# Kernel tuning notes

Hardware: AMD Instinct MI355X
Metric: run time of the kernel (lower is better)

Reference implementation:

```python
import jax, jax.numpy as jnp
import numpy as np

N = 100000   # nodes
E = 1000000  # edges
H = 64       # hidden_channels
METAPATH = (0, 1, 2)


def setup_inputs() -> dict:
    key = jax.random.key(0)
    ks = jax.random.split(key, 32)
    inp = {
        "x": jax.random.normal(ks[0], (N, 2 * H), dtype=jnp.float32),
        "edge_index": jax.random.randint(ks[1], (2, E), 0, N, dtype=jnp.int64),
        "edge_type": jax.random.randint(ks[2], (E,), 0, 3, dtype=jnp.int64),
    }
    # layer 0: in = 2H, layers 1,2: in = H; torch Linear weight is [out, in]
    ki = 3
    for l, in_dim in enumerate([2 * H, H, H]):
        for wname in ["wl", "w0", "w1"]:
            inp[f"{wname}{l}"] = jax.random.normal(ks[ki], (H, in_dim), dtype=jnp.float32) * 0.05
            ki += 1
            inp[f"{wname[0]}b{wname[1]}{l}"] = jnp.zeros((H,), dtype=jnp.float32)
    return inp


def _layer(x_in, h, mask, src, dst, wl, bl, w0, b0, w1, b1):
    # aggr='add', flow='target_to_source': agg[src[e]] += h[dst[e]] for masked edges
    msg = jnp.where(mask[:, None], h[dst], jnp.zeros((), h.dtype))  # [E, H]
    agg = jax.ops.segment_sum(msg, src, num_segments=N)             # [N, H]
    return agg @ wl.T + bl + h @ w0.T + b0 + x_in @ w1.T + b1


def reference(x, edge_index, edge_type,
              wl0, wbl0, w00, wb00, w10, wb10,
              wl1, wbl1, w01, wb01, w11, wb11,
              wl2, wbl2, w02, wb02, w12, wb12):
    src, dst = edge_index[0], edge_index[1]
    params = [
        (wl0, wbl0, w00, wb00, w10, wb10),
        (wl1, wbl1, w01, wb01, w11, wb11),
        (wl2, wbl2, w02, wb02, w12, wb12),
    ]
    h = x
    for i, rel in enumerate(METAPATH):
        mask = edge_type == rel
        x_in = x if i == 0 else h
        h = jax.nn.relu(_layer(x_in, h, mask, src, dst, *params[i]))
        # F.dropout with training=False is identity (eval mode reference)
    return h
```

## Files before the change

### kernel.cpp

```cpp
#include <hip/hip_runtime.h>
#include <cstdint>
#include <cstddef>

#define NNODES 100000
#define NEDGES 1000000
#define NREL 3
#define RN (NREL * NNODES)
#define EPB 2048
#define SCAN_BLOCKS ((RN + EPB - 1) / EPB)


__global__ __launch_bounds__(256) void hist_kernel(
    const int* __restrict__ srcv, const int* __restrict__ ety, int* __restrict__ cnt)
{
    const int e = (int)(blockIdx.x * 256 + threadIdx.x);
    if (e < NEDGES) atomicAdd(&cnt[ety[e] * NNODES + srcv[e]], 1);
}

__global__ __launch_bounds__(256) void scan_reduce(
    const int* __restrict__ cnt, int* __restrict__ bsum)
{
    __shared__ int sd[256];
    const int t = (int)threadIdx.x;
    const int base = (int)blockIdx.x * EPB + t * 8;
    int s = 0;
    #pragma unroll
    for (int i = 0; i < 8; ++i)
        if (base + i < RN) s += cnt[base + i];
    sd[t] = s;
    __syncthreads();
    for (int st = 128; st > 0; st >>= 1) {
        if (t < st) sd[t] += sd[t + st];
        __syncthreads();
    }
    if (t == 0) bsum[blockIdx.x] = sd[0];
}

__global__ __launch_bounds__(256) void scan_blocksums(int* __restrict__ bsum, int nb)
{
    __shared__ int buf0[256], buf1[256];
    const int t = (int)threadIdx.x;
    buf0[t] = (t < nb) ? bsum[t] : 0;
    __syncthreads();
    int* a = buf0; int* b = buf1;
    for (int st = 1; st < 256; st <<= 1) {
        int v = a[t];
        if (t >= st) v += a[t - st];
        b[t] = v;
        __syncthreads();
        int* tmp = a; a = b; b = tmp;
    }
    if (t < nb) bsum[t] = (t == 0) ? 0 : a[t - 1];
}

__global__ __launch_bounds__(256) void scan_final(
    const int* __restrict__ cnt, const int* __restrict__ bsum,
    int* __restrict__ off, int* __restrict__ wptr)
{
    __shared__ int buf0[256], buf1[256];
    const int t = (int)threadIdx.x;
    const int base = (int)blockIdx.x * EPB + t * 8;
    int v[8];
    int tot = 0;
    #pragma unroll
    for (int i = 0; i < 8; ++i) {
        v[i] = (base + i < RN) ? cnt[base + i] : 0;
        tot += v[i];
    }
    buf0[t] = tot;
    __syncthreads();
    int* a = buf0; int* b = buf1;
    for (int st = 1; st < 256; st <<= 1) {
        int s = a[t];
        if (t >= st) s += a[t - st];
        b[t] = s;
        __syncthreads();
        int* tmp = a; a = b; b = tmp;
    }
    int o = bsum[blockIdx.x] + ((t == 0) ? 0 : a[t - 1]);
    #pragma unroll
    for (int i = 0; i < 8; ++i) {
        if (base + i < RN) { off[base + i] = o; wptr[base + i] = o; }
        o += v[i];
    }
    if (blockIdx.x == 0 && t == 0) off[RN] = NEDGES;
}

__global__ __launch_bounds__(256) void fill_kernel(
    const int* __restrict__ srcv, const int* __restrict__ dstv,
    const int* __restrict__ ety, int* __restrict__ wptr, int* __restrict__ ebuf)
{
    const int e = (int)(blockIdx.x * 256 + threadIdx.x);
    if (e < NEDGES) {
        const int pos = atomicAdd(&wptr[ety[e] * NNODES + srcv[e]], 1);
        ebuf[pos] = dstv[e];
    }
}

template<int K>
__global__ __launch_bounds__(256) void gather_kernel(
    const int* __restrict__ off, const int* __restrict__ ebuf,
    const float* __restrict__ h, float* __restrict__ agg, int rel)
{
    const int lane = (int)(threadIdx.x & 63);
    const int wid  = (int)((blockIdx.x * blockDim.x + threadIdx.x) >> 6);
    const int nw   = (int)((gridDim.x * blockDim.x) >> 6);
    const int* o = off + rel * NNODES;
    for (int n = wid; n < NNODES; n += nw) {
        const int s  = o[n];
        const int e1 = o[n + 1];
        float a0 = 0.f, a1 = 0.f;
        for (int j = s; j < e1; ++j) {
            const int d = ebuf[j];
            const float* hr = h + (size_t)d * K;
            a0 += hr[lane];
            if (K == 128) a1 += hr[64 + lane];
        }
        agg[(size_t)n * K + lane] = a0;
        if (K == 128) agg[(size_t)n * K + 64 + lane] = a1;
    }
}

template<int K>
__global__ __launch_bounds__(256) void dense_gemm(
    const float* __restrict__ A1, const float* __restrict__ A2,
    const float* __restrict__ W1, const float* __restrict__ W2a, const float* __restrict__ W2b,
    const float* __restrict__ B1, const float* __restrict__ B2, const float* __restrict__ B3,
    float* __restrict__ out, int nNodes)
{
    __shared__ float As[16][64];
    __shared__ float Ws[16][64];

    const int t  = (int)threadIdx.x;
    const int tx = t & 15;
    const int ty = t >> 4;
    const int n0 = (int)blockIdx.x * 64;

    const int srow = t >> 2;
    const int skk  = (t & 3) * 4;

    float4 acc[4];
    #pragma unroll
    for (int i = 0; i < 4; ++i) acc[i] = make_float4(0.f, 0.f, 0.f, 0.f);

    const int KC = K / 16;
    const int nA = n0 + srow;

    #pragma unroll 1
    for (int c = 0; c < 2 * KC; ++c) {
        const bool first = (c < KC);
        const int k0 = (first ? c : c - KC) * 16;

        float4 av = make_float4(0.f, 0.f, 0.f, 0.f);
        if (nA < nNodes) {
            const float* Ab = first ? A1 : A2;
            av = *(const float4*)(Ab + (size_t)nA * K + k0 + skk);
        }
        float4 wv;
        if (first) {
            wv = *(const float4*)(W1 + (size_t)srow * K + k0 + skk);
        } else {
            const float4 a = *(const float4*)(W2a + (size_t)srow * K + k0 + skk);
            const float4 b = *(const float4*)(W2b + (size_t)srow * K + k0 + skk);
            wv = make_float4(a.x + b.x, a.y + b.y, a.z + b.z, a.w + b.w);
        }

        __syncthreads();
        As[skk + 0][srow] = av.x; As[skk + 1][srow] = av.y;
        As[skk + 2][srow] = av.z; As[skk + 3][srow] = av.w;
        Ws[skk + 0][srow] = wv.x; Ws[skk + 1][srow] = wv.y;
        Ws[skk + 2][srow] = wv.z; Ws[skk + 3][srow] = wv.w;
        __syncthreads();

        #pragma unroll
        for (int k = 0; k < 16; ++k) {
            const float4 a4 = *(const float4*)&As[k][ty * 4];
            const float4 w4 = *(const float4*)&Ws[k][tx * 4];
            acc[0].x = fmaf(a4.x, w4.x, acc[0].x); acc[0].y = fmaf(a4.x, w4.y, acc[0].y);
            acc[0].z = fmaf(a4.x, w4.z, acc[0].z); acc[0].w = fmaf(a4.x, w4.w, acc[0].w);
            acc[1].x = fmaf(a4.y, w4.x, acc[1].x); acc[1].y = fmaf(a4.y, w4.y, acc[1].y);
            acc[1].z = fmaf(a4.y, w4.z, acc[1].z); acc[1].w = fmaf(a4.y, w4.w, acc[1].w);
            acc[2].x = fmaf(a4.z, w4.x, acc[2].x); acc[2].y = fmaf(a4.z, w4.y, acc[2].y);
            acc[2].z = fmaf(a4.z, w4.z, acc[2].z); acc[2].w = fmaf(a4.z, w4.w, acc[2].w);
            acc[3].x = fmaf(a4.w, w4.x, acc[3].x); acc[3].y = fmaf(a4.w, w4.y, acc[3].y);
            acc[3].z = fmaf(a4.w, w4.z, acc[3].z); acc[3].w = fmaf(a4.w, w4.w, acc[3].w);
        }
    }

    const float4 b1 = *(const float4*)(B1 + tx * 4);
    const float4 b2 = *(const float4*)(B2 + tx * 4);
    const float4 b3 = *(const float4*)(B3 + tx * 4);
    const float4 bias = make_float4(b1.x + b2.x + b3.x, b1.y + b2.y + b3.y,
                                    b1.z + b2.z + b3.z, b1.w + b2.w + b3.w);
    #pragma unroll
    for (int i = 0; i < 4; ++i) {
        const int n = n0 + ty * 4 + i;
        if (n < nNodes) {
            float4 r = make_float4(acc[i].x + bias.x, acc[i].y + bias.y,
                                   acc[i].z + bias.z, acc[i].w + bias.w);
            r.x = r.x > 0.f ? r.x : 0.f;
            r.y = r.y > 0.f ? r.y : 0.f;
            r.z = r.z > 0.f ? r.z : 0.f;
            r.w = r.w > 0.f ? r.w : 0.f;
            *(float4*)(out + (size_t)n * 64 + tx * 4) = r;
        }
    }
}

extern "C" void kernel_launch(void* const* d_in, const int* in_sizes, int n_in,
                              void* d_out, int out_size, void* d_ws, size_t ws_size,
                              hipStream_t stream)
{
    const float* x    = (const float*)d_in[0];
    const int*   eidx = (const int*)d_in[1];
    const int*   ety  = (const int*)d_in[2];
    const int*   srcv = eidx;
    const int*   dstv = eidx + NEDGES;

    const float* wl0 = (const float*)d_in[3];
    const float* bl0 = (const float*)d_in[4];
    const float* w00 = (const float*)d_in[5];
    const float* b00 = (const float*)d_in[6];
    const float* w10 = (const float*)d_in[7];
    const float* b10 = (const float*)d_in[8];

    const float* wl1 = (const float*)d_in[9];
    const float* bl1 = (const float*)d_in[10];
    const float* w01 = (const float*)d_in[11];
    const float* b01 = (const float*)d_in[12];
    const float* w11 = (const float*)d_in[13];
    const float* b11 = (const float*)d_in[14];

    const float* wl2 = (const float*)d_in[15];
    const float* bl2 = (const float*)d_in[16];
    const float* w02 = (const float*)d_in[17];
    const float* b02 = (const float*)d_in[18];
    const float* w12 = (const float*)d_in[19];
    const float* b12 = (const float*)d_in[20];

    char* p = (char*)d_ws;
    auto alloc = [&](size_t bytes) {
        char* r = p;
        p += (bytes + 255) & ~(size_t)255;
        return r;
    };
    int* cnt  = (int*)alloc((size_t)RN * 4);
    int* off  = (int*)alloc((size_t)(RN + 1) * 4);
    int* wptr = (int*)alloc((size_t)RN * 4);
    int* bsum = (int*)alloc(1024);
    int* ebuf = (int*)alloc((size_t)NEDGES * 4);
    float* aggA = (float*)alloc((size_t)NNODES * 64 * sizeof(float));
    float* aggB = (float*)alloc((size_t)NNODES * 64 * sizeof(float));
    float* h1 = (float*)d_out;

    const int edgeGrid = (NEDGES + 255) / 256;
    const int gemmGrid = (NNODES + 63) / 64;

    hipMemsetAsync(cnt, 0, (size_t)RN * 4, stream);
    hist_kernel<<<edgeGrid, 256, 0, stream>>>(srcv, ety, cnt);
    scan_reduce<<<SCAN_BLOCKS, 256, 0, stream>>>(cnt, bsum);
    scan_blocksums<<<1, 256, 0, stream>>>(bsum, SCAN_BLOCKS);
    scan_final<<<SCAN_BLOCKS, 256, 0, stream>>>(cnt, bsum, off, wptr);
    fill_kernel<<<edgeGrid, 256, 0, stream>>>(srcv, dstv, ety, wptr, ebuf);

    gather_kernel<128><<<4096, 256, 0, stream>>>(off, ebuf, x, aggA, 0);
    dense_gemm<128><<<gemmGrid, 256, 0, stream>>>(aggA, x, wl0, w00, w10,
                                                  bl0, b00, b10, h1, NNODES);

    gather_kernel<64><<<4096, 256, 0, stream>>>(off, ebuf, h1, aggA, 1);
    dense_gemm<64><<<gemmGrid, 256, 0, stream>>>(aggA, h1, wl1, w01, w11,
                                                 bl1, b01, b11, aggB, NNODES);

    gather_kernel<64><<<4096, 256, 0, stream>>>(off, ebuf, aggB, aggA, 2);
    dense_gemm<64><<<gemmGrid, 256, 0, stream>>>(aggA, aggB, wl2, w02, w12,
                                                 bl2, b02, b12, (float*)d_out, NNODES);
}
```

Baseline: 501.1 us.

## Fuse neighbor gather into per-layer GEMM kernel with shared-memory aggregation tile

```diff
diff --git a/kernel.cpp b/kernel.cpp
--- a/kernel.cpp
+++ b/kernel.cpp
@@ -98,44 +98,59 @@
 }
 
 template<int K>
-__global__ __launch_bounds__(256) void gather_kernel(
+__global__ __launch_bounds__(256) void fused_layer(
     const int* __restrict__ off, const int* __restrict__ ebuf,
-    const float* __restrict__ h, float* __restrict__ agg, int rel)
-{
-    const int lane = (int)(threadIdx.x & 63);
-    const int wid  = (int)((blockIdx.x * blockDim.x + threadIdx.x) >> 6);
-    const int nw   = (int)((gridDim.x * blockDim.x) >> 6);
-    const int* o = off + rel * NNODES;
-    for (int n = wid; n < NNODES; n += nw) {
-        const int s  = o[n];
-        const int e1 = o[n + 1];
-        float a0 = 0.f, a1 = 0.f;
-        for (int j = s; j < e1; ++j) {
-            const int d = ebuf[j];
-            const float* hr = h + (size_t)d * K;
-            a0 += hr[lane];
-            if (K == 128) a1 += hr[64 + lane];
-        }
-        agg[(size_t)n * K + lane] = a0;
-        if (K == 128) agg[(size_t)n * K + 64 + lane] = a1;
-    }
-}
-
-template<int K>
-__global__ __launch_bounds__(256) void dense_gemm(
-    const float* __restrict__ A1, const float* __restrict__ A2,
+    const float* __restrict__ h,
     const float* __restrict__ W1, const float* __restrict__ W2a, const float* __restrict__ W2b,
     const float* __restrict__ B1, const float* __restrict__ B2, const float* __restrict__ B3,
-    float* __restrict__ out, int nNodes)
-{
+    float* __restrict__ out, int rel, int nNodes)
+{
+    constexpr int PAD = (K == 128) ? 132 : 68;
+    __shared__ float Agg[64][PAD];
     __shared__ float As[16][64];
     __shared__ float Ws[16][64];
 
-    const int t  = (int)threadIdx.x;
+    const int t    = (int)threadIdx.x;
+    const int lane = t & 63;
+    const int wv   = t >> 6;
+    const int n0   = (int)blockIdx.x * 64;
+
+    const int* o = off + rel * NNODES;
+    #pragma unroll 1
+    for (int ii = 0; ii < 8; ++ii) {
+        const int nlA = wv * 16 + ii;
+        const int nlB = nlA + 8;
+        const int nA = n0 + nlA, nB = n0 + nlB;
+        int jA = 0, eA = 0, jB = 0, eB = 0;
+        if (nA < nNodes) { jA = o[nA]; eA = o[nA + 1]; }
+        if (nB < nNodes) { jB = o[nB]; eB = o[nB + 1]; }
+        float a0A = 0.f, a1A = 0.f, a0B = 0.f, a1B = 0.f;
+        while (jA < eA && jB < eB) {
+            const int dA = ebuf[jA++];
+            const int dB = ebuf[jB++];
+            const float* hA = h + (size_t)dA * K;
+            const float* hB = h + (size_t)dB * K;
+            a0A += hA[lane]; a0B += hB[lane];
+            if (K == 128) { a1A += hA[64 + lane]; a1B += hB[64 + lane]; }
+        }
+        while (jA < eA) {
+            const float* hA = h + (size_t)ebuf[jA++] * K;
+            a0A += hA[lane];
+            if (K == 128) a1A += hA[64 + lane];
+        }
+        while (jB < eB) {
+            const float* hB = h + (size_t)ebuf[jB++] * K;
+            a0B += hB[lane];
+            if (K == 128) a1B += hB[64 + lane];
+        }
+        Agg[nlA][lane] = a0A;
+        Agg[nlB][lane] = a0B;
+        if (K == 128) { Agg[nlA][64 + lane] = a1A; Agg[nlB][64 + lane] = a1B; }
+    }
+    __syncthreads();
+
     const int tx = t & 15;
     const int ty = t >> 4;
-    const int n0 = (int)blockIdx.x * 64;
-
     const int srow = t >> 2;
     const int skk  = (t & 3) * 4;
 
@@ -147,29 +162,47 @@
     const int nA = n0 + srow;
 
     #pragma unroll 1
-    for (int c = 0; c < 2 * KC; ++c) {
-        const bool first = (c < KC);
-        const int k0 = (first ? c : c - KC) * 16;
-
+    for (int c = 0; c < KC; ++c) {
+        const float4 wv4 = *(const float4*)(W1 + (size_t)srow * K + c * 16 + skk);
+        __syncthreads();
+        Ws[skk + 0][srow] = wv4.x; Ws[skk + 1][srow] = wv4.y;
+        Ws[skk + 2][srow] = wv4.z; Ws[skk + 3][srow] = wv4.w;
+        __syncthreads();
+        #pragma unroll
+        for (int k4 = 0; k4 < 4; ++k4) {
+            const float4 w0 = *(const float4*)&Ws[k4 * 4 + 0][tx * 4];
+            const float4 w1 = *(const float4*)&Ws[k4 * 4 + 1][tx * 4];
+            const float4 w2 = *(const float4*)&Ws[k4 * 4 + 2][tx * 4];
+            const float4 w3 = *(const float4*)&Ws[k4 * 4 + 3][tx * 4];
+            #pragma unroll
+            for (int i = 0; i < 4; ++i) {
+                const float4 a4 = *(const float4*)&Agg[ty * 4 + i][c * 16 + k4 * 4];
+                acc[i].x = fmaf(a4.x, w0.x, acc[i].x); acc[i].y = fmaf(a4.x, w0.y, acc[i].y);
+                acc[i].z = fmaf(a4.x, w0.z, acc[i].z); acc[i].w = fmaf(a4.x, w0.w, acc[i].w);
+                acc[i].x = fmaf(a4.y, w1.x, acc[i].x); acc[i].y = fmaf(a4.y, w1.y, acc[i].y);
+                acc[i].z = fmaf(a4.y, w1.z, acc[i].z); acc[i].w = fmaf(a4.y, w1.w, acc[i].w);
+                acc[i].x = fmaf(a4.z, w2.x, acc[i].x); acc[i].y = fmaf(a4.z, w2.y, acc[i].y);
+                acc[i].z = fmaf(a4.z, w2.z, acc[i].z); acc[i].w = fmaf(a4.z, w2.w, acc[i].w);
+                acc[i].x = fmaf(a4.w, w3.x, acc[i].x); acc[i].y = fmaf(a4.w, w3.y, acc[i].y);
+                acc[i].z = fmaf(a4.w, w3.z, acc[i].z); acc[i].w = fmaf(a4.w, w3.w, acc[i].w);
+            }
+        }
+    }
+
+    #pragma unroll 1
+    for (int c = 0; c < KC; ++c) {
+        const int k0 = c * 16;
         float4 av = make_float4(0.f, 0.f, 0.f, 0.f);
-        if (nA < nNodes) {
-            const float* Ab = first ? A1 : A2;
-            av = *(const float4*)(Ab + (size_t)nA * K + k0 + skk);
-        }
-        float4 wv;
-        if (first) {
-            wv = *(const float4*)(W1 + (size_t)srow * K + k0 + skk);
-        } else {
-            const float4 a = *(const float4*)(W2a + (size_t)srow * K + k0 + skk);
-            const float4 b = *(const float4*)(W2b + (size_t)srow * K + k0 + skk);
-            wv = make_float4(a.x + b.x, a.y + b.y, a.z + b.z, a.w + b.w);
-        }
+        if (nA < nNodes) av = *(const float4*)(h + (size_t)nA * K + k0 + skk);
+        const float4 a = *(const float4*)(W2a + (size_t)srow * K + k0 + skk);
+        const float4 b = *(const float4*)(W2b + (size_t)srow * K + k0 + skk);
+        const float4 wv4 = make_float4(a.x + b.x, a.y + b.y, a.z + b.z, a.w + b.w);
 
         __syncthreads();
         As[skk + 0][srow] = av.x; As[skk + 1][srow] = av.y;
         As[skk + 2][srow] = av.z; As[skk + 3][srow] = av.w;
-        Ws[skk + 0][srow] = wv.x; Ws[skk + 1][srow] = wv.y;
-        Ws[skk + 2][srow] = wv.z; Ws[skk + 3][srow] = wv.w;
+        Ws[skk + 0][srow] = wv4.x; Ws[skk + 1][srow] = wv4.y;
+        Ws[skk + 2][srow] = wv4.z; Ws[skk + 3][srow] = wv4.w;
         __syncthreads();
 
         #pragma unroll
@@ -249,12 +282,11 @@
     int* wptr = (int*)alloc((size_t)RN * 4);
     int* bsum = (int*)alloc(1024);
     int* ebuf = (int*)alloc((size_t)NEDGES * 4);
-    float* aggA = (float*)alloc((size_t)NNODES * 64 * sizeof(float));
-    float* aggB = (float*)alloc((size_t)NNODES * 64 * sizeof(float));
+    float* h2 = (float*)alloc((size_t)NNODES * 64 * sizeof(float));
     float* h1 = (float*)d_out;
 
-    const int edgeGrid = (NEDGES + 255) / 256;
-    const int gemmGrid = (NNODES + 63) / 64;
+    const int edgeGrid  = (NEDGES + 255) / 256;
+    const int fusedGrid = (NNODES + 63) / 64;
 
     hipMemsetAsync(cnt, 0, (size_t)RN * 4, stream);
     hist_kernel<<<edgeGrid, 256, 0, stream>>>(srcv, ety, cnt);
@@ -263,15 +295,10 @@
     scan_final<<<SCAN_BLOCKS, 256, 0, stream>>>(cnt, bsum, off, wptr);
     fill_kernel<<<edgeGrid, 256, 0, stream>>>(srcv, dstv, ety, wptr, ebuf);
 
-    gather_kernel<128><<<4096, 256, 0, stream>>>(off, ebuf, x, aggA, 0);
-    dense_gemm<128><<<gemmGrid, 256, 0, stream>>>(aggA, x, wl0, w00, w10,
-                                                  bl0, b00, b10, h1, NNODES);
-
-    gather_kernel<64><<<4096, 256, 0, stream>>>(off, ebuf, h1, aggA, 1);
-    dense_gemm<64><<<gemmGrid, 256, 0, stream>>>(aggA, h1, wl1, w01, w11,
-                                                 bl1, b01, b11, aggB, NNODES);
-
-    gather_kernel<64><<<4096, 256, 0, stream>>>(off, ebuf, aggB, aggA, 2);
-    dense_gemm<64><<<gemmGrid, 256, 0, stream>>>(aggA, aggB, wl2, w02, w12,
-                                                 bl2, b02, b12, (float*)d_out, NNODES);
-}
+    fused_layer<128><<<fusedGrid, 256, 0, stream>>>(off, ebuf, x, wl0, w00, w10,
+                                                    bl0, b00, b10, h1, 0, NNODES);
+    fused_layer<64><<<fusedGrid, 256, 0, stream>>>(off, ebuf, h1, wl1, w01, w11,
+                                                   bl1, b01, b11, h2, 1, NNODES);
+    fused_layer<64><<<fusedGrid, 256, 0, stream>>>(off, ebuf, h2, wl2, w02, w12,
+                                                   bl2, b02, b12, (float*)d_out, 2, NNODES);
+}
```

After: 520.5 us. +3.9%, slower.
